# Optimization experiments

Hardware: AMD Instinct MI355X
Metric: run time of the kernel (lower is better)

Reference implementation:

```python
import jax, jax.numpy as jnp
from jax import lax
import numpy as np

MSS = 1448.0
MAX_RTT = 0.01
B, S = 2048, 4096


def setup_inputs() -> dict:
    key = jax.random.key(0)
    k1, k2, k3, k4 = jax.random.split(key, 4)
    # packet lengths in [0, 1500) bytes so bursts aggregate past MSS=1448
    x = jax.random.uniform(k1, (B, S), jnp.float32) * 1500.0
    mask = jax.random.uniform(k2, (B, S)) < 0.1
    scale = 0.00094557476340694
    d_exp = 1e-6 + scale * jax.random.exponential(k3, (B, S), jnp.float32)
    delays = jnp.where(mask, jnp.float32(0.21), d_exp)
    # per-burst RTT samples, indexed by the burst-start packet position
    rtts = jax.random.uniform(k4, (B, S), jnp.float32) * MAX_RTT
    return {"x": x, "delays": delays, "rtts": rtts}


def _simulate_row(x, delays, rtts):
    # x, delays, rtts: [S]
    S_ = x.shape[0]

    def step(carry, inp):
        active, new_burst, r = carry
        xj, dj, rj = inp
        # outer-while check only at burst start: stop forever if x[j] <= 0
        active = jnp.where(new_burst, active & (xj > 0), active)
        r = jnp.where(new_burst, rj, r)
        r_next = r - dj  # inner while: RTT -= delays[j]
        burst_end = active & (r_next <= 0)
        start_flag = new_burst & active
        return (active, burst_end, r_next), (active, start_flag)

    init = (jnp.bool_(True), jnp.bool_(True), jnp.float32(0.0))
    _, (consumed, start_flag) = lax.scan(step, init, (x, delays, rtts))

    # per-burst buffered byte count: segment-sum of consumed packet lengths
    burst_id = jnp.clip(jnp.cumsum(start_flag.astype(jnp.int32)) - 1, 0, S_ - 1)
    buf = jax.ops.segment_sum(jnp.where(consumed, x, 0.0), burst_id, num_segments=S_)

    # `while buf > MSS` emits ceil(buf/MSS)-1 full segments, then remainder
    n_full = jnp.maximum(jnp.ceil(buf / MSS).astype(jnp.int32) - 1, 0)
    rem = buf - n_full.astype(x.dtype) * MSS
    has_rem = rem > 0
    count = n_full + has_rem.astype(jnp.int32)
    starts = jnp.cumsum(count) - count  # exclusive cumsum: output offset per burst
    ends = starts + n_full

    # difference-array trick: positions in [starts, ends) get MSS (OOB drops == truncation)
    diff = (jnp.zeros(S_, jnp.int32)
            .at[starts].add(1, mode='drop')
            .at[ends].add(-1, mode='drop'))
    cover = jnp.cumsum(diff) > 0
    out = jnp.where(cover, jnp.float32(MSS), jnp.float32(0.0))

    # remainder goes right after the MSS run of its burst
    rem_pos = jnp.where(has_rem, ends, S_)  # S_ -> dropped
    out = out.at[rem_pos].set(rem, mode='drop')
    return out


def reference(x, delays, rtts):
    out = jax.vmap(_simulate_row)(x, delays, rtts)  # [B, S]
    return out[..., None]  # unsqueeze(-1) -> [B, S, 1]
```

## Files before the change

### kernel.cpp

```cpp
#include <hip/hip_runtime.h>
#include <math.h>


#define S_LEN 4096
#define BLOCK 512
#define PER   8
#define MSSF  1448.0f

#define OFF_A    0
#define OFF_JB   8208
#define OFF_MENT 16416
#define OFF_WS   17440
#define SMEM_SZ  17472

__global__ __launch_bounds__(BLOCK, 6) void traffic_kernel(
    const float* __restrict__ gx,
    const float* __restrict__ gd,
    const float* __restrict__ gr,
    float* __restrict__ gout)
{
    __shared__ __align__(16) unsigned char smem[SMEM_SZ];
    float*          s_dly  = (float*)(smem + OFF_A);
    unsigned short* s_jA   = (unsigned short*)(smem + OFF_A);
    unsigned short* s_jB   = (unsigned short*)(smem + OFF_JB);
    int*            s_diff = (int*)(smem + OFF_A);
    float*          s_out  = (float*)(smem + OFF_A);
    unsigned short* s_ment = (unsigned short*)(smem + OFF_MENT);
    int*            s_ws   = (int*)(smem + OFF_WS);

    const int tid = threadIdx.x;
    const int sb  = tid << 3;
    const size_t rowoff = (size_t)blockIdx.x * S_LEN;
    const float* px = gx + rowoff;
    const float* pd = gd + rowoff;
    const float* pr = gr + rowoff;

    float xreg[PER];
    float rt[PER];
    {
        float4 xa = *(const float4*)(px + sb);
        float4 xb = *(const float4*)(px + sb + 4);
        xreg[0]=xa.x; xreg[1]=xa.y; xreg[2]=xa.z; xreg[3]=xa.w;
        xreg[4]=xb.x; xreg[5]=xb.y; xreg[6]=xb.z; xreg[7]=xb.w;
        float4 ra = *(const float4*)(pr + sb);
        float4 rb = *(const float4*)(pr + sb + 4);
        rt[0]=ra.x; rt[1]=ra.y; rt[2]=ra.z; rt[3]=ra.w;
        rt[4]=rb.x; rt[5]=rb.y; rt[6]=rb.z; rt[7]=rb.w;
    }
    {
        const float4* pd4 = (const float4*)pd;
        float4* s4 = (float4*)s_dly;
        for (int q = tid; q < S_LEN / 4; q += BLOCK) s4[q] = pd4[q];
        if (tid < 8) s_dly[S_LEN + tid] = 1.0e30f;
    }
    __syncthreads();

    float dl[16];
    {
        const float4* dv = (const float4*)(s_dly + sb);
        float4 a0 = dv[0], a1 = dv[1], a2 = dv[2], a3 = dv[3];
        dl[0]=a0.x;  dl[1]=a0.y;  dl[2]=a0.z;  dl[3]=a0.w;
        dl[4]=a1.x;  dl[5]=a1.y;  dl[6]=a1.z;  dl[7]=a1.w;
        dl[8]=a2.x;  dl[9]=a2.y;  dl[10]=a2.z; dl[11]=a2.w;
        dl[12]=a3.x; dl[13]=a3.y; dl[14]=a3.z; dl[15]=a3.w;
    }

    unsigned surv = 0;
    float rsv[PER];
    int nx8[PER];
#pragma unroll
    for (int i = 0; i < PER; ++i) {
        float r1 = rt[i] - dl[i];
        float r2 = r1 - dl[i + 1];
        float r3 = r2 - dl[i + 2];
        float r4 = r3 - dl[i + 3];
        float r5 = r4 - dl[i + 4];
        float r6 = r5 - dl[i + 5];
        float r7 = r6 - dl[i + 6];
        float r8 = r7 - dl[i + 7];
        int c = (r1 > 0.0f) + (r2 > 0.0f) + (r3 > 0.0f) + (r4 > 0.0f) +
                (r5 > 0.0f) + (r6 > 0.0f) + (r7 > 0.0f) + (r8 > 0.0f);
        rsv[i] = r8;
        int nx = sb + i + c + 1;
        if (nx > S_LEN) nx = S_LEN;
        nx8[i] = nx;
        if (c == 8) surv |= 1u << i;
    }

    while (surv) {
        int i = __ffs(surv) - 1;
        surv &= surv - 1;
        float rr = rsv[0];
#pragma unroll
        for (int ii = 1; ii < PER; ++ii) rr = (i == ii) ? rsv[ii] : rr;
        int j = sb + i + 8;
        int nx;
        while (true) {
            float e0 = s_dly[j],     e1 = s_dly[j + 1];
            float e2 = s_dly[j + 2], e3 = s_dly[j + 3];
            float e4 = s_dly[j + 4], e5 = s_dly[j + 5];
            float e6 = s_dly[j + 6], e7 = s_dly[j + 7];
            float q1 = rr - e0;
            float q2 = q1 - e1;
            float q3 = q2 - e2;
            float q4 = q3 - e3;
            float q5 = q4 - e4;
            float q6 = q5 - e5;
            float q7 = q6 - e6;
            float q8 = q7 - e7;
            int c2 = (q1 > 0.0f) + (q2 > 0.0f) + (q3 > 0.0f) + (q4 > 0.0f) +
                     (q5 > 0.0f) + (q6 > 0.0f) + (q7 > 0.0f) + (q8 > 0.0f);
            if (c2 < 8) { nx = j + c2 + 1; break; }
            j += 8;
            rr = q8;
        }
        if (nx > S_LEN) nx = S_LEN;
#pragma unroll
        for (int ii = 0; ii < PER; ++ii) nx8[ii] = (ii == i) ? nx : nx8[ii];
    }
    __syncthreads();

    int own[PER];
    unsigned long long rel = 0x8ull << 32;
    {
#pragma unroll
        for (int i = 0; i < PER; ++i)
            if (!(xreg[i] > 0.0f)) nx8[i] = S_LEN;
        int ee[PER];
#pragma unroll
        for (int i = PER - 1; i >= 0; --i) {
            int v = nx8[i];
            int e = v;
#pragma unroll
            for (int j2 = i + 1; j2 < PER; ++j2)
                if (v == sb + j2) e = ee[j2];
            ee[i] = e;
        }
        uint4 pk;
        pk.x = (unsigned)ee[0] | ((unsigned)ee[1] << 16);
        pk.y = (unsigned)ee[2] | ((unsigned)ee[3] << 16);
        pk.z = (unsigned)ee[4] | ((unsigned)ee[5] << 16);
        pk.w = (unsigned)ee[6] | ((unsigned)ee[7] << 16);
        *(uint4*)&s_jA[sb] = pk;
#pragma unroll
        for (int i = 0; i < PER; ++i) {
            int r = nx8[i] - sb; if (r > 8) r = 8;
            rel |= (unsigned long long)r << (i << 2);
        }
#pragma unroll
        for (int i = 0; i < PER; ++i) own[i] = ee[i];
    }
    if (tid == 0) { s_jA[4096] = (unsigned short)4096; s_jB[4096] = (unsigned short)4096; }
    s_ment[tid] = (tid == 0) ? (unsigned short)1 : (unsigned short)0;
    __syncthreads();

    {
        unsigned short* ja = s_jA;
        unsigned short* jb = s_jB;
        for (int k = 0; k < 9; ++k) {
            int ent = (int)s_ment[tid];
            int q = -1;
            if (ent) {
                int e = (int)ja[ent - 1];
                if (e < S_LEN) q = e;
            }
            if (k < 8) {
                int nv[PER];
#pragma unroll
                for (int i = 0; i < PER; ++i) nv[i] = (int)ja[own[i]];
                if (q >= 0) s_ment[q >> 3] = (unsigned short)(q + 1);
                uint4 pk;
                pk.x = (unsigned)nv[0] | ((unsigned)nv[1] << 16);
                pk.y = (unsigned)nv[2] | ((unsigned)nv[3] << 16);
                pk.z = (unsigned)nv[4] | ((unsigned)nv[5] << 16);
                pk.w = (unsigned)nv[6] | ((unsigned)nv[7] << 16);
                *(uint4*)&jb[sb] = pk;
#pragma unroll
                for (int i = 0; i < PER; ++i) own[i] = nv[i];
            } else {
                if (q >= 0) s_ment[q >> 3] = (unsigned short)(q + 1);
            }
            __syncthreads();
            unsigned short* t = ja; ja = jb; jb = t;
        }
    }

    unsigned lm = 0;
    {
        int ent = (int)s_ment[tid];
        if (ent) {
            int p = ent - 1 - sb;
#pragma unroll
            for (int s = 0; s < PER; ++s) {
                lm |= (p < 8) ? (1u << p) : 0u;
                p = (int)((rel >> (p << 2)) & 15ull);
            }
        }
    }

    int   nf8[PER];
    float rem8[PER];
    unsigned use = 0;
    int tsum = 0;
#pragma unroll
    for (int i = 0; i < PER; ++i) {
        int nf = 0;
        float rem = 0.0f;
        if ((lm >> i) & 1u) {
            float xp = xreg[i];
            if (xp > 0.0f) {
                use |= 1u << i;
                int e = nx8[i];
                int upper = e - sb;
                float sum = xp;
#pragma unroll
                for (int jj = i + 1; jj < PER; ++jj)
                    sum += (jj < upper) ? xreg[jj] : 0.0f;
                for (int j = sb + PER; j < e; ++j) sum += px[j];
                nf = (int)ceilf(sum / MSSF) - 1; if (nf < 0) nf = 0;
                rem = sum - (float)nf * MSSF;
                tsum += nf + (rem > 0.0f ? 1 : 0);
            }
        }
        nf8[i] = nf;
        rem8[i] = rem;
    }

    {
        int4* d4 = (int4*)s_diff;
        int4 z; z.x = z.y = z.z = z.w = 0;
        d4[tid] = z;
        d4[tid + 512] = z;
    }
    int texcl;
    {
        int lane = tid & 63, wv = tid >> 6;
        int v = tsum;
        for (int off = 1; off < 64; off <<= 1) {
            int u = __shfl_up(v, off, 64);
            if (lane >= off) v += u;
        }
        if (lane == 63) s_ws[wv] = v;
        __syncthreads();
        int woff = 0;
        for (int w = 0; w < wv; ++w) woff += s_ws[w];
        texcl = woff + v - tsum;
    }

    {
        int o = texcl;
#pragma unroll
        for (int i = 0; i < PER; ++i) {
            if ((use >> i) & 1u) {
                int nf = nf8[i];
                if (nf > 0) {
                    if (o < S_LEN) atomicAdd(&s_diff[o], 1);
                    int e2 = o + nf;
                    if (e2 < S_LEN) atomicAdd(&s_diff[e2], -1);
                }
                o += nf + (rem8[i] > 0.0f ? 1 : 0);
            }
        }
    }
    __syncthreads();

    {
        int4 a = *(int4*)&s_diff[sb];
        int4 b = *(int4*)&s_diff[sb + 4];
        int v0 = a.x,      v1 = v0 + a.y, v2 = v1 + a.z, v3 = v2 + a.w;
        int v4 = v3 + b.x, v5 = v4 + b.y, v6 = v5 + b.z, v7 = v6 + b.w;
        int T = v7;
        int lane = tid & 63, wv = tid >> 6;
        int sc = T;
        for (int off = 1; off < 64; off <<= 1) {
            int u = __shfl_up(sc, off, 64);
            if (lane >= off) sc += u;
        }
        if (lane == 63) s_ws[wv] = sc;
        __syncthreads();
        int basev = 0;
        for (int w = 0; w < wv; ++w) basev += s_ws[w];
        basev += sc - T;
        float4 fa, fb;
        fa.x = (basev + v0 > 0) ? MSSF : 0.0f;
        fa.y = (basev + v1 > 0) ? MSSF : 0.0f;
        fa.z = (basev + v2 > 0) ? MSSF : 0.0f;
        fa.w = (basev + v3 > 0) ? MSSF : 0.0f;
        fb.x = (basev + v4 > 0) ? MSSF : 0.0f;
        fb.y = (basev + v5 > 0) ? MSSF : 0.0f;
        fb.z = (basev + v6 > 0) ? MSSF : 0.0f;
        fb.w = (basev + v7 > 0) ? MSSF : 0.0f;
        *(float4*)&s_out[sb]     = fa;
        *(float4*)&s_out[sb + 4] = fb;
    }
    __syncthreads();

    {
        int o = texcl;
#pragma unroll
        for (int i = 0; i < PER; ++i) {
            if ((use >> i) & 1u) {
                int nf = nf8[i];
                float rem = rem8[i];
                int rp = o + nf;
                if (rem > 0.0f && rp < S_LEN) s_out[rp] = rem;
                o += nf + (rem > 0.0f ? 1 : 0);
            }
        }
    }
    __syncthreads();

    {
        float4* po4 = (float4*)(gout + rowoff);
        const float4* so4 = (const float4*)s_out;
        po4[tid]       = so4[tid];
        po4[tid + 512] = so4[tid + 512];
    }
}

extern "C" void kernel_launch(void* const* d_in, const int* in_sizes, int n_in,
                              void* d_out, int out_size, void* d_ws, size_t ws_size,
                              hipStream_t stream) {
    const float* x      = (const float*)d_in[0];
    const float* delays = (const float*)d_in[1];
    const float* rtts   = (const float*)d_in[2];
    float* out = (float*)d_out;
    int rows = in_sizes[0] / S_LEN;
    traffic_kernel<<<rows, BLOCK, 0, stream>>>(x, delays, rtts, out);
}
```

Baseline: 170.3 us.

## Load delays directly into registers, drop shared staging and extend prefilter window

```diff
diff --git a/kernel.cpp b/kernel.cpp
--- a/kernel.cpp
+++ b/kernel.cpp
@@ -13,14 +13,15 @@
 #define OFF_WS   17440
 #define SMEM_SZ  17472
 
-__global__ __launch_bounds__(BLOCK, 6) void traffic_kernel(
+#define EXT(K) ((K) < 16 ? dla[(K)] : dlb[(K) - 16])
+
+__global__ __launch_bounds__(BLOCK, 8) void traffic_kernel(
     const float* __restrict__ gx,
     const float* __restrict__ gd,
     const float* __restrict__ gr,
     float* __restrict__ gout)
 {
     __shared__ __align__(16) unsigned char smem[SMEM_SZ];
-    float*          s_dly  = (float*)(smem + OFF_A);
     unsigned short* s_jA   = (unsigned short*)(smem + OFF_A);
     unsigned short* s_jB   = (unsigned short*)(smem + OFF_JB);
     int*            s_diff = (int*)(smem + OFF_A);
@@ -47,22 +48,28 @@
         rt[0]=ra.x; rt[1]=ra.y; rt[2]=ra.z; rt[3]=ra.w;
         rt[4]=rb.x; rt[5]=rb.y; rt[6]=rb.z; rt[7]=rb.w;
     }
-    {
-        const float4* pd4 = (const float4*)pd;
-        float4* s4 = (float4*)s_dly;
-        for (int q = tid; q < S_LEN / 4; q += BLOCK) s4[q] = pd4[q];
-        if (tid < 8) s_dly[S_LEN + tid] = 1.0e30f;
-    }
-    __syncthreads();
-
-    float dl[16];
-    {
-        const float4* dv = (const float4*)(s_dly + sb);
+    float dla[16], dlb[8];
+    if (sb + 16 <= S_LEN) {
+        const float4* dv = (const float4*)(pd + sb);
         float4 a0 = dv[0], a1 = dv[1], a2 = dv[2], a3 = dv[3];
-        dl[0]=a0.x;  dl[1]=a0.y;  dl[2]=a0.z;  dl[3]=a0.w;
-        dl[4]=a1.x;  dl[5]=a1.y;  dl[6]=a1.z;  dl[7]=a1.w;
-        dl[8]=a2.x;  dl[9]=a2.y;  dl[10]=a2.z; dl[11]=a2.w;
-        dl[12]=a3.x; dl[13]=a3.y; dl[14]=a3.z; dl[15]=a3.w;
+        dla[0]=a0.x;  dla[1]=a0.y;  dla[2]=a0.z;  dla[3]=a0.w;
+        dla[4]=a1.x;  dla[5]=a1.y;  dla[6]=a1.z;  dla[7]=a1.w;
+        dla[8]=a2.x;  dla[9]=a2.y;  dla[10]=a2.z; dla[11]=a2.w;
+        dla[12]=a3.x; dla[13]=a3.y; dla[14]=a3.z; dla[15]=a3.w;
+    } else {
+#pragma unroll
+        for (int q = 0; q < 16; ++q)
+            dla[q] = (sb + q < S_LEN) ? pd[sb + q] : 1.0e30f;
+    }
+    if (sb + 24 <= S_LEN) {
+        const float4* dv = (const float4*)(pd + sb + 16);
+        float4 b0 = dv[0], b1 = dv[1];
+        dlb[0]=b0.x; dlb[1]=b0.y; dlb[2]=b0.z; dlb[3]=b0.w;
+        dlb[4]=b1.x; dlb[5]=b1.y; dlb[6]=b1.z; dlb[7]=b1.w;
+    } else {
+#pragma unroll
+        for (int q = 0; q < 8; ++q)
+            dlb[q] = (sb + 16 + q < S_LEN) ? pd[sb + 16 + q] : 1.0e30f;
     }
 
     unsigned surv = 0;
@@ -70,14 +77,14 @@
     int nx8[PER];
 #pragma unroll
     for (int i = 0; i < PER; ++i) {
-        float r1 = rt[i] - dl[i];
-        float r2 = r1 - dl[i + 1];
-        float r3 = r2 - dl[i + 2];
-        float r4 = r3 - dl[i + 3];
-        float r5 = r4 - dl[i + 4];
-        float r6 = r5 - dl[i + 5];
-        float r7 = r6 - dl[i + 6];
-        float r8 = r7 - dl[i + 7];
+        float r1 = rt[i] - dla[i];
+        float r2 = r1 - dla[i + 1];
+        float r3 = r2 - dla[i + 2];
+        float r4 = r3 - dla[i + 3];
+        float r5 = r4 - dla[i + 4];
+        float r6 = r5 - dla[i + 5];
+        float r7 = r6 - dla[i + 6];
+        float r8 = r7 - dla[i + 7];
         int c = (r1 > 0.0f) + (r2 > 0.0f) + (r3 > 0.0f) + (r4 > 0.0f) +
                 (r5 > 0.0f) + (r6 > 0.0f) + (r7 > 0.0f) + (r8 > 0.0f);
         rsv[i] = r8;
@@ -87,19 +94,53 @@
         if (c == 8) surv |= 1u << i;
     }
 
-    while (surv) {
-        int i = __ffs(surv) - 1;
-        surv &= surv - 1;
+    unsigned surv2 = 0;
+    if (surv) {
+#pragma unroll
+        for (int i = 0; i < PER; ++i) {
+            if ((surv >> i) & 1u) {
+                float rr = rsv[i];
+                float q1 = rr - EXT(i + 8);
+                float q2 = q1 - EXT(i + 9);
+                float q3 = q2 - EXT(i + 10);
+                float q4 = q3 - EXT(i + 11);
+                float q5 = q4 - EXT(i + 12);
+                float q6 = q5 - EXT(i + 13);
+                float q7 = q6 - EXT(i + 14);
+                float q8 = q7 - EXT(i + 15);
+                int c2 = (q1 > 0.0f) + (q2 > 0.0f) + (q3 > 0.0f) + (q4 > 0.0f) +
+                         (q5 > 0.0f) + (q6 > 0.0f) + (q7 > 0.0f) + (q8 > 0.0f);
+                rsv[i] = q8;
+                if (c2 == 8) {
+                    surv2 |= 1u << i;
+                } else {
+                    int nx = sb + i + 8 + c2 + 1;
+                    if (nx > S_LEN) nx = S_LEN;
+                    nx8[i] = nx;
+                }
+            }
+        }
+    }
+
+    while (surv2) {
+        int i = __ffs(surv2) - 1;
+        surv2 &= surv2 - 1;
         float rr = rsv[0];
 #pragma unroll
         for (int ii = 1; ii < PER; ++ii) rr = (i == ii) ? rsv[ii] : rr;
-        int j = sb + i + 8;
+        int j = sb + i + 16;
         int nx;
         while (true) {
-            float e0 = s_dly[j],     e1 = s_dly[j + 1];
-            float e2 = s_dly[j + 2], e3 = s_dly[j + 3];
-            float e4 = s_dly[j + 4], e5 = s_dly[j + 5];
-            float e6 = s_dly[j + 6], e7 = s_dly[j + 7];
+            float e0 = 1.0e30f, e1 = 1.0e30f, e2 = 1.0e30f, e3 = 1.0e30f;
+            float e4 = 1.0e30f, e5 = 1.0e30f, e6 = 1.0e30f, e7 = 1.0e30f;
+            if (j     < S_LEN) e0 = pd[j];
+            if (j + 1 < S_LEN) e1 = pd[j + 1];
+            if (j + 2 < S_LEN) e2 = pd[j + 2];
+            if (j + 3 < S_LEN) e3 = pd[j + 3];
+            if (j + 4 < S_LEN) e4 = pd[j + 4];
+            if (j + 5 < S_LEN) e5 = pd[j + 5];
+            if (j + 6 < S_LEN) e6 = pd[j + 6];
+            if (j + 7 < S_LEN) e7 = pd[j + 7];
             float q1 = rr - e0;
             float q2 = q1 - e1;
             float q3 = q2 - e2;
@@ -118,7 +159,6 @@
 #pragma unroll
         for (int ii = 0; ii < PER; ++ii) nx8[ii] = (ii == i) ? nx : nx8[ii];
     }
-    __syncthreads();
 
     int own[PER];
     unsigned long long rel = 0x8ull << 32;
@@ -167,7 +207,10 @@
             if (k < 8) {
                 int nv[PER];
 #pragma unroll
-                for (int i = 0; i < PER; ++i) nv[i] = (int)ja[own[i]];
+                for (int i = 0; i < PER; ++i) {
+                    int o = own[i];
+                    nv[i] = (o >= S_LEN) ? S_LEN : (int)ja[o];
+                }
                 if (q >= 0) s_ment[q >> 3] = (unsigned short)(q + 1);
                 uint4 pk;
                 pk.x = (unsigned)nv[0] | ((unsigned)nv[1] << 16);
@@ -216,7 +259,14 @@
 #pragma unroll
                 for (int jj = i + 1; jj < PER; ++jj)
                     sum += (jj < upper) ? xreg[jj] : 0.0f;
-                for (int j = sb + PER; j < e; ++j) sum += px[j];
+                int j = sb + PER;
+                for (; j + 8 <= e; j += 8) {
+                    float4 a = *(const float4*)(px + j);
+                    float4 b = *(const float4*)(px + j + 4);
+                    sum += a.x; sum += a.y; sum += a.z; sum += a.w;
+                    sum += b.x; sum += b.y; sum += b.z; sum += b.w;
+                }
+                for (; j < e; ++j) sum += px[j];
                 nf = (int)ceilf(sum / MSSF) - 1; if (nf < 0) nf = 0;
                 rem = sum - (float)nf * MSSF;
                 tsum += nf + (rem > 0.0f ? 1 : 0);
@@ -242,8 +292,16 @@
         }
         if (lane == 63) s_ws[wv] = v;
         __syncthreads();
+        int4 w0 = *(const int4*)s_ws;
+        int4 w1 = *(const int4*)(s_ws + 4);
         int woff = 0;
-        for (int w = 0; w < wv; ++w) woff += s_ws[w];
+        woff += (wv > 0) ? w0.x : 0;
+        woff += (wv > 1) ? w0.y : 0;
+        woff += (wv > 2) ? w0.z : 0;
+        woff += (wv > 3) ? w0.w : 0;
+        woff += (wv > 4) ? w1.x : 0;
+        woff += (wv > 5) ? w1.y : 0;
+        woff += (wv > 6) ? w1.z : 0;
         texcl = woff + v - tsum;
     }
 
@@ -278,8 +336,16 @@
         }
         if (lane == 63) s_ws[wv] = sc;
         __syncthreads();
+        int4 w0 = *(const int4*)s_ws;
+        int4 w1 = *(const int4*)(s_ws + 4);
         int basev = 0;
-        for (int w = 0; w < wv; ++w) basev += s_ws[w];
+        basev += (wv > 0) ? w0.x : 0;
+        basev += (wv > 1) ? w0.y : 0;
+        basev += (wv > 2) ? w0.z : 0;
+        basev += (wv > 3) ? w0.w : 0;
+        basev += (wv > 4) ? w1.x : 0;
+        basev += (wv > 5) ? w1.y : 0;
+        basev += (wv > 6) ? w1.z : 0;
         basev += sc - T;
         float4 fa, fb;
         fa.x = (basev + v0 > 0) ? MSSF : 0.0f;
```

New measurement: 169.0 us. About the same (-0.8%).
